# Optimization experiments

Hardware: AMD Instinct MI355X
Metric: run time of the kernel (lower is better)

## Reference

```python
import jax, jax.numpy as jnp
import numpy as np

B, S, H = 4, 2048, 1024
NH, HD = 16, 64
LN_EPS = 1e-5


def _l2norm(x, axis=-1, eps=1e-12):
    n = jnp.sqrt(jnp.sum(x * x, axis=axis, keepdims=True))
    return x / jnp.maximum(n, eps)


def setup_inputs() -> dict:
    key = jax.random.key(0)
    ks = jax.random.split(key, 10)
    sd = 0.02
    x = jax.random.normal(ks[0], (B, S, H), jnp.float32)
    Wq = jax.random.normal(ks[1], (H, H), jnp.float32) * sd
    Wk = jax.random.normal(ks[2], (H, H), jnp.float32) * sd
    Wv = jax.random.normal(ks[3], (H, H), jnp.float32) * sd
    Wa = jax.random.normal(ks[4], (NH, H), jnp.float32) * sd
    ba = jnp.zeros((NH,), jnp.float32)
    Wb = jax.random.normal(ks[5], (NH, H), jnp.float32) * sd
    bb = jnp.zeros((NH,), jnp.float32)
    Wg = jax.random.normal(ks[6], (H, H), jnp.float32) * sd
    Wo = jax.random.normal(ks[7], (H, H), jnp.float32) * sd
    ln_g = jnp.ones((H,), jnp.float32)
    ln_b = jnp.zeros((H,), jnp.float32)
    return {"x": x, "Wq": Wq, "Wk": Wk, "Wv": Wv, "Wa": Wa, "ba": ba,
            "Wb": Wb, "bb": bb, "Wg": Wg, "Wo": Wo, "ln_g": ln_g, "ln_b": ln_b}


def _forward(x, Wq, Wk, Wv, Wa, ba, Wb, bb, Wg, Wo, ln_g, ln_b):
    q = _l2norm((x @ Wq.T).reshape(B, S, NH, HD))  # [B,S,nh,hd]
    k = _l2norm((x @ Wk.T).reshape(B, S, NH, HD))
    v = jax.nn.silu(x @ Wv.T).reshape(B, S, NH, HD)
    alpha = jax.nn.sigmoid(x @ Wa.T + ba)  # [B,S,nh]
    beta = jax.nn.sigmoid(x @ Wb.T + bb)   # [B,S,nh]

    def step(state, inp):
        a_t, b_t, k_t, v_t, q_t = inp  # a,b: [B,nh]; k,v,q: [B,nh,hd]
        a_ = a_t[:, :, None, None]
        b_ = b_t[:, :, None, None]
        kk = k_t[..., :, None] * k_t[..., None, :]  # [B,nh,hd,hd]
        state = a_ * state * (1.0 - b_ * kk) + b_ * (v_t[..., :, None] * k_t[..., None, :])
        out_t = jnp.sum(state * q_t[..., None, :], axis=-1)  # [B,nh,hd]
        return state, out_t

    # time-major xs for scan
    xs = (jnp.moveaxis(alpha, 1, 0), jnp.moveaxis(beta, 1, 0),
          jnp.moveaxis(k, 1, 0), jnp.moveaxis(v, 1, 0), jnp.moveaxis(q, 1, 0))
    state0 = jnp.zeros((B, NH, HD, HD), x.dtype)
    _, outs = jax.lax.scan(step, state0, xs)  # [S,B,nh,hd]
    out = jnp.moveaxis(outs, 0, 1).reshape(B, S, H)

    # LayerNorm over total_dim
    mu = jnp.mean(out, axis=-1, keepdims=True)
    var = jnp.var(out, axis=-1, keepdims=True)
    out = (out - mu) / jnp.sqrt(var + LN_EPS) * ln_g + ln_b

    out = out * jax.nn.silu(x @ Wg.T)
    return out @ Wo.T


def reference(x, Wq, Wk, Wv, Wa, ba, Wb, bb, Wg, Wo, ln_g, ln_b):
    return _forward(x, Wq, Wk, Wv, Wa, ba, Wb, bb, Wg, Wo, ln_g, ln_b)
```

## Files before the change

kernel.cpp:

```cpp
#include <hip/hip_runtime.h>

typedef unsigned short u16;
typedef __bf16 bf16x8 __attribute__((ext_vector_type(8)));
typedef float f32x4 __attribute__((ext_vector_type(4)));

constexpr int Bq  = 4;
constexpr int Sq  = 2048;
constexpr int Hq  = 1024;
constexpr int NHq = 16;
constexpr int HDq = 64;
constexpr int CCH = 16;
constexpr int LCH = 128;

constexpr size_t OFF_WB = 0;
constexpr size_t OFF_XB = 10485760;
constexpr size_t OFF_Q  = 27262976;
constexpr size_t OFF_K  = 60817408;
constexpr size_t OFF_V  = 94371840;
constexpr size_t OFF_G  = 127926272;
constexpr size_t OFF_AL = 161480704;
constexpr size_t OFF_BE = 162004992;
constexpr size_t OFF_P  = 162529280;
constexpr size_t OFF_O  = 179306496;

__device__ __forceinline__ u16 f2bf(float f) {
  unsigned u = __float_as_uint(f);
  u += 0x7fffu + ((u >> 16) & 1u);
  return (u16)(u >> 16);
}
__device__ __forceinline__ float sigmoidf_(float x) { return 1.f / (1.f + __expf(-x)); }

__device__ __forceinline__ void async16(const void* g, void* l) {
  __builtin_amdgcn_global_load_lds((const __attribute__((address_space(1))) void*)g,
                                   (__attribute__((address_space(3))) void*)l, 16, 0, 0);
}

__global__ __launch_bounds__(256) void cvt_x_kernel(const float* __restrict__ in, u16* __restrict__ outp) {
  const size_t i = ((size_t)blockIdx.x * 256 + threadIdx.x) * 4;
  float4 f = *(const float4*)(in + i);
  ushort4 u; u.x = f2bf(f.x); u.y = f2bf(f.y); u.z = f2bf(f.z); u.w = f2bf(f.w);
  *(ushort4*)(outp + i) = u;
}

__global__ __launch_bounds__(256) void cvt_w_kernel(const float* __restrict__ w0, const float* __restrict__ w1,
    const float* __restrict__ w2, const float* __restrict__ w3, const float* __restrict__ w4,
    u16* __restrict__ outp) {
  const int z = blockIdx.z;
  const float* src = (z == 0) ? w0 : (z == 1) ? w1 : (z == 2) ? w2 : (z == 3) ? w3 : w4;
  const size_t i = ((size_t)blockIdx.x * 256 + threadIdx.x) * 4;
  float4 f = *(const float4*)(src + i);
  ushort4 u; u.x = f2bf(f.x); u.y = f2bf(f.y); u.z = f2bf(f.z); u.w = f2bf(f.w);
  *(ushort4*)(outp + (size_t)z * (1024 * 1024) + i) = u;
}

__global__ __launch_bounds__(256) void cvt_ab_kernel(const float* __restrict__ Wa, const float* __restrict__ Wb,
    u16* __restrict__ outp) {
  const size_t i = ((size_t)blockIdx.x * 256 + threadIdx.x) * 4;
  const int row = (int)(i >> 10);
  const float* src = (row < 16) ? (Wa + i) : (Wb + i - 16 * 1024);
  float4 f = *(const float4*)src;
  ushort4 u; u.x = f2bf(f.x); u.y = f2bf(f.y); u.z = f2bf(f.z); u.w = f2bf(f.w);
  *(ushort4*)(outp + i) = u;
}

__global__ __launch_bounds__(256) void ab_gemm(const u16* __restrict__ A, const u16* __restrict__ Wab,
    float* __restrict__ al, float* __restrict__ be, const float* __restrict__ ba, const float* __restrict__ bb) {
  const int tid = threadIdx.x, wv = tid >> 6, lane = tid & 63;
  const int l15 = lane & 15, qd = lane >> 4;
  const int m0 = blockIdx.x * 128 + wv * 32;
  const u16* gA = A + (size_t)m0 * 1024 + qd * 8;
  const u16* gB = Wab + (size_t)l15 * 1024 + qd * 8;
  f32x4 acc[2][2] = {};
#pragma unroll 4
  for (int kt = 0; kt < 1024; kt += 32) {
    bf16x8 a0 = *(const bf16x8*)(gA + (size_t)l15 * 1024 + kt);
    bf16x8 a1 = *(const bf16x8*)(gA + (size_t)(16 + l15) * 1024 + kt);
    bf16x8 b0 = *(const bf16x8*)(gB + kt);
    bf16x8 b1 = *(const bf16x8*)(gB + 16 * 1024 + kt);
    acc[0][0] = __builtin_amdgcn_mfma_f32_16x16x32_bf16(a0, b0, acc[0][0], 0, 0, 0);
    acc[0][1] = __builtin_amdgcn_mfma_f32_16x16x32_bf16(a0, b1, acc[0][1], 0, 0, 0);
    acc[1][0] = __builtin_amdgcn_mfma_f32_16x16x32_bf16(a1, b0, acc[1][0], 0, 0, 0);
    acc[1][1] = __builtin_amdgcn_mfma_f32_16x16x32_bf16(a1, b1, acc[1][1], 0, 0, 0);
  }
  const float bav = ba[l15], bbv = bb[l15];
#pragma unroll
  for (int mi = 0; mi < 2; ++mi) {
    const int row = m0 + mi * 16 + qd * 4;
#pragma unroll
    for (int r = 0; r < 4; ++r) {
      al[(size_t)(row + r) * 16 + l15] = sigmoidf_(acc[mi][0][r] + bav);
      be[(size_t)(row + r) * 16 + l15] = sigmoidf_(acc[mi][1][r] + bbv);
    }
  }
}

__device__ __forceinline__ void lda4(bf16x8 af[4][2], const u16* LA, int wr, int mh, int l15, int qd, int l7) {
#pragma unroll
  for (int i = 0; i < 4; ++i)
#pragma unroll
    for (int kk = 0; kk < 2; ++kk)
      af[i][kk] = *(const bf16x8*)(LA + (wr * 128 + mh * 64 + i * 16 + l15) * 64 + (((kk * 4 + qd) ^ l7) * 8));
}
__device__ __forceinline__ void ldb2(bf16x8 bf[2][2], const u16* LB, int wc, int nh, int l15, int qd, int l7) {
#pragma unroll
  for (int j = 0; j < 2; ++j)
#pragma unroll
    for (int kk = 0; kk < 2; ++kk)
      bf[j][kk] = *(const bf16x8*)(LB + (wc * 64 + nh * 32 + j * 16 + l15) * 64 + (((kk * 4 + qd) ^ l7) * 8));
}
__device__ __forceinline__ void mm16(f32x4 acc[8][4], const bf16x8 af[4][2], const bf16x8 bf[2][2], int mh, int nh) {
#pragma unroll
  for (int i = 0; i < 4; ++i)
#pragma unroll
    for (int j = 0; j < 2; ++j) {
      f32x4 c = acc[mh * 4 + i][nh * 2 + j];
      c = __builtin_amdgcn_mfma_f32_16x16x32_bf16(af[i][0], bf[j][0], c, 0, 0, 0);
      c = __builtin_amdgcn_mfma_f32_16x16x32_bf16(af[i][1], bf[j][1], c, 0, 0, 0);
      acc[mh * 4 + i][nh * 2 + j] = c;
    }
}
__device__ __forceinline__ void stageH(u16* LD, int bufp, int mat, int h, const u16* gRow0, int kElem,
                                       int rr, int sl8, int wv) {
  const u16* s0 = gRow0 + (size_t)(h * 128 + rr) * 1024 + kElem + sl8;
  u16* d = LD + bufp * 32768 + mat * 16384 + h * 8192 + wv * 512;
  async16(s0, d);
  async16(s0 + (size_t)(64 * 1024), d + 4096);
}

template<int S1, int S2, int VM>
__device__ __forceinline__ void tile16(u16* LD, int bp, int kt,
    const u16* gA, const u16* gB, f32x4 acc[8][4], bf16x8 af[4][2], bf16x8 bf0[2][2], bf16x8 bf1[2][2],
    int wr, int wc, int l15, int qd, int l7, int rr, int sl8, int wv) {
  const u16* LA = LD + bp * 32768;
  const u16* LB = LA + 16384;
  lda4(af, LA, wr, 0, l15, qd, l7);
  ldb2(bf0, LB, wc, 0, l15, qd, l7);
  if (S1) stageH(LD, bp ^ 1, 0, 0, gA, (kt + 1) * 64, rr, sl8, wv);
  __builtin_amdgcn_s_barrier();
  asm volatile("s_waitcnt lgkmcnt(0)" ::: "memory");
  __builtin_amdgcn_sched_barrier(0);
  __builtin_amdgcn_s_setprio(1);
  mm16(acc, af, bf0, 0, 0);
  __builtin_amdgcn_s_setprio(0);
  __builtin_amdgcn_s_barrier();
  ldb2(bf1, LB, wc, 1, l15, qd, l7);
  if (S1) stageH(LD, bp ^ 1, 0, 1, gA, (kt + 1) * 64, rr, sl8, wv);
  __builtin_amdgcn_s_barrier();
  asm volatile("s_waitcnt lgkmcnt(0)" ::: "memory");
  __builtin_amdgcn_sched_barrier(0);
  __builtin_amdgcn_s_setprio(1);
  mm16(acc, af, bf1, 0, 1);
  __builtin_amdgcn_s_setprio(0);
  __builtin_amdgcn_s_barrier();
  lda4(af, LA, wr, 1, l15, qd, l7);
  if (S2) stageH(LD, bp, 1, 0, gB, (kt + 2) * 64, rr, sl8, wv);
  __builtin_amdgcn_s_barrier();
  asm volatile("s_waitcnt lgkmcnt(0)" ::: "memory");
  __builtin_amdgcn_sched_barrier(0);
  __builtin_amdgcn_s_setprio(1);
  mm16(acc, af, bf0, 1, 0);
  __builtin_amdgcn_s_setprio(0);
  __builtin_amdgcn_s_barrier();
  if (S2) stageH(LD, bp, 1, 1, gB, (kt + 2) * 64, rr, sl8, wv);
  __builtin_amdgcn_s_barrier();
  __builtin_amdgcn_sched_barrier(0);
  __builtin_amdgcn_s_setprio(1);
  mm16(acc, af, bf1, 1, 1);
  __builtin_amdgcn_s_setprio(0);
  if (VM == 4) asm volatile("s_waitcnt vmcnt(4)" ::: "memory");
  else if (VM == 0) asm volatile("s_waitcnt vmcnt(0)" ::: "memory");
  __builtin_amdgcn_s_barrier();
}

__global__ __launch_bounds__(512, 2) void gemm256(const u16* __restrict__ A, const u16* __restrict__ Wall,
    float* __restrict__ Cq, float* __restrict__ Ck, float* __restrict__ Cv, float* __restrict__ Cg,
    int mode) {
  __shared__ __align__(16) u16 Lds[65536];
  u16* LD = &Lds[0];
  const int tid = threadIdx.x;
  const int wv = tid >> 6, lane = tid & 63;
  const int l15 = lane & 15, qd = lane >> 4, l7 = l15 & 7;
  const int wr = wv >> 2, wc = wv & 3;
  const int rr = tid >> 3, sl8 = ((tid & 7) ^ (rr & 7)) * 8;

  int mx, ny, z;
  const u16* Wm;
  if (mode == 0) {
    const int job = ((blockIdx.x & 7) << 4) + (blockIdx.x >> 3);
    mx = job & 31; ny = job >> 5; z = 0; Wm = Wall;
  } else {
    const int job = ((blockIdx.x & 7) << 6) + (blockIdx.x >> 3);
    mx = job & 31; ny = (job >> 5) & 3; z = job >> 7;
    Wm = Wall + (size_t)z * (1024 * 1024);
  }
  const int m0 = mx * 256, n0 = ny * 256;
  const u16* gA = A + (size_t)m0 * 1024;
  const u16* gB = Wm + (size_t)n0 * 1024;

  f32x4 acc[8][4] = {};
  bf16x8 af[4][2], bf0[2][2], bf1[2][2];

  stageH(LD, 0, 0, 0, gA, 0,  rr, sl8, wv);
  stageH(LD, 0, 0, 1, gA, 0,  rr, sl8, wv);
  stageH(LD, 0, 1, 0, gB, 0,  rr, sl8, wv);
  stageH(LD, 0, 1, 1, gB, 0,  rr, sl8, wv);
  stageH(LD, 1, 1, 0, gB, 64, rr, sl8, wv);
  stageH(LD, 1, 1, 1, gB, 64, rr, sl8, wv);
  asm volatile("s_waitcnt vmcnt(4)" ::: "memory");
  __builtin_amdgcn_s_barrier();

#pragma unroll 1
  for (int t2 = 0; t2 < 7; ++t2) {
    tile16<1, 1, 4>(LD, 0, 2 * t2,     gA, gB, acc, af, bf0, bf1, wr, wc, l15, qd, l7, rr, sl8, wv);
    tile16<1, 1, 4>(LD, 1, 2 * t2 + 1, gA, gB, acc, af, bf0, bf1, wr, wc, l15, qd, l7, rr, sl8, wv);
  }
  tile16<1, 0, 0>(LD, 0, 14, gA, gB, acc, af, bf0, bf1, wr, wc, l15, qd, l7, rr, sl8, wv);
  tile16<0, 0, -1>(LD, 1, 15, gA, gB, acc, af, bf0, bf1, wr, wc, l15, qd, l7, rr, sl8, wv);

  if (mode == 1 && z <= 1) {
#pragma unroll
    for (int mi = 0; mi < 8; ++mi)
#pragma unroll
      for (int r = 0; r < 4; ++r) {
        float ss = acc[mi][0][r] * acc[mi][0][r] + acc[mi][1][r] * acc[mi][1][r]
                 + acc[mi][2][r] * acc[mi][2][r] + acc[mi][3][r] * acc[mi][3][r];
        ss += __shfl_xor(ss, 1); ss += __shfl_xor(ss, 2);
        ss += __shfl_xor(ss, 4); ss += __shfl_xor(ss, 8);
        const float rn = 1.f / fmaxf(sqrtf(ss), 1e-12f);
        acc[mi][0][r] *= rn; acc[mi][1][r] *= rn; acc[mi][2][r] *= rn; acc[mi][3][r] *= rn;
      }
  } else if (mode == 1 && z == 2) {
#pragma unroll
    for (int mi = 0; mi < 8; ++mi)
#pragma unroll
      for (int ni = 0; ni < 4; ++ni)
#pragma unroll
        for (int r = 0; r < 4; ++r)
          acc[mi][ni][r] = acc[mi][ni][r] * sigmoidf_(acc[mi][ni][r]);
  }
  float* C = (mode == 0) ? Cq : ((z == 0) ? Cq : (z == 1) ? Ck : (z == 2) ? Cv : Cg);
#pragma unroll
  for (int mi = 0; mi < 8; ++mi) {
    const int row = m0 + wr * 128 + mi * 16 + qd * 4;
#pragma unroll
    for (int ni = 0; ni < 4; ++ni) {
      const int col = n0 + wc * 64 + ni * 16 + l15;
#pragma unroll
      for (int r = 0; r < 4; ++r)
        C[(size_t)(row + r) * 1024 + col] = acc[mi][ni][r];
    }
  }
}

struct ScanLds1 { float kb[2][16 * 64]; float vb[2][16 * 64]; float ab[2][32]; };
struct ScanLds2 { float kb[2][16 * 64]; float qb[2][16 * 64]; float vb[2][16 * 64]; float ab[2][32]; };

__global__ __launch_bounds__(256, 4) void scan_p1(const float* __restrict__ k, const float* __restrict__ v,
    const float* __restrict__ al, const float* __restrict__ be,
    float* __restrict__ P, float* __restrict__ Q) {
  __shared__ ScanLds1 L;
  const int tid = threadIdx.x, wv = tid >> 6, lane = tid & 63;
  const int bh = blockIdx.x >> 4, c = blockIdx.x & 15;
  const int b = bh >> 4, h = bh & 15;
  const int rg = lane >> 3, cg = lane & 7;
  const int r0 = wv * 16 + rg * 2, c8 = cg * 8;
  const size_t base0 = ((size_t)(b * Sq + c * LCH)) * 1024 + h * 64;
  const size_t ab0   = ((size_t)(b * Sq + c * LCH)) * 16 + h;
  const int tokw = lane >> 4, seg = lane & 15;
  auto stage = [&](int tile, int bi) {
    #pragma unroll
    for (int j = 0; j < 2; ++j) {
      const int job = wv * 2 + j;
      const int arr = job >> 2, i = job & 3;
      const float* src = arr ? v : k;
      float* dst = arr ? &L.vb[bi][i * 256] : &L.kb[bi][i * 256];
      async16(src + base0 + (size_t)(tile * 16 + i * 4 + tokw) * 1024 + seg * 4, dst);
    }
    if (wv == 0 && lane < 32) {
      const int w16 = lane >> 4, tt = lane & 15;
      const float* s = w16 ? be : al;
      L.ab[bi][w16 * 16 + tt] = s[ab0 + (size_t)(tile * 16 + tt) * 16];
    }
  };
  float Pr[16], Qr[16];
  #pragma unroll
  for (int i = 0; i < 16; ++i) { Pr[i] = 1.f; Qr[i] = 0.f; }
  stage(0, 0);
  for (int tile = 0; tile < 8; ++tile) {
    __syncthreads();
    if (tile < 7) stage(tile + 1, (tile + 1) & 1);
    const int bi = tile & 1;
    const float* kbp = L.kb[bi];
    const float* vbp = L.vb[bi];
    const float* abp = L.ab[bi];
    #pragma unroll 4
    for (int tt = 0; tt < 16; ++tt) {
      const float a = abp[tt], bt = abp[16 + tt];
      float4 kcv0 = *(const float4*)(kbp + tt * 64 + c8);
      float4 kcv1 = *(const float4*)(kbp + tt * 64 + c8 + 4);
      float2 krvv = *(const float2*)(kbp + tt * 64 + r0);
      float2 vrvv = *(const float2*)(vbp + tt * 64 + r0);
      const float kcv[8] = {kcv0.x, kcv0.y, kcv0.z, kcv0.w, kcv1.x, kcv1.y, kcv1.z, kcv1.w};
      const float krv[2] = {krvv.x, krvv.y};
      const float vrv[2] = {vrvv.x, vrvv.y};
      const float abt = a * bt;
      float c1[2], c2[2];
      #pragma unroll
      for (int i = 0; i < 2; ++i) { c1[i] = abt * krv[i]; c2[i] = bt * vrv[i]; }
      #pragma unroll
      for (int i = 0; i < 2; ++i)
        #pragma unroll
        for (int j = 0; j < 8; ++j) {
          const int e = i * 8 + j;
          const float A = fmaf(-c1[i], kcv[j], a);
          Qr[e] = fmaf(A, Qr[e], c2[i] * kcv[j]);
          Pr[e] *= A;
        }
    }
  }
  const size_t pbase = ((size_t)bh * CCH + c) * 4096 + (size_t)c8;
  #pragma unroll
  for (int i = 0; i < 2; ++i) {
    const size_t pi = pbase + (size_t)(r0 + i) * 64;
    *(float4*)(P + pi)     = make_float4(Pr[i*8],   Pr[i*8+1], Pr[i*8+2], Pr[i*8+3]);
    *(float4*)(P + pi + 4) = make_float4(Pr[i*8+4], Pr[i*8+5], Pr[i*8+6], Pr[i*8+7]);
    *(float4*)(Q + pi)     = make_float4(Qr[i*8],   Qr[i*8+1], Qr[i*8+2], Qr[i*8+3]);
    *(float4*)(Q + pi + 4) = make_float4(Qr[i*8+4], Qr[i*8+5], Qr[i*8+6], Qr[i*8+7]);
  }
}

__global__ __launch_bounds__(256) void scan_comb(float* __restrict__ P, const float* __restrict__ Q) {
  const int g = blockIdx.x * 256 + threadIdx.x;
  const int elem = g & 4095;
  const int bh = g >> 12;
  float s = 0.f;
  #pragma unroll
  for (int c = 0; c < CCH; ++c) {
    const size_t idx = ((size_t)bh * CCH + c) * 4096 + elem;
    const float p = P[idx], qq = Q[idx];
    P[idx] = s;
    s = fmaf(p, s, qq);
  }
}

__global__ __launch_bounds__(256, 4) void scan_p2(const float* __restrict__ q, const float* __restrict__ k,
    const float* __restrict__ v, const float* __restrict__ al, const float* __restrict__ be,
    const float* __restrict__ Pini, float* __restrict__ o) {
  __shared__ ScanLds2 L;
  const int tid = threadIdx.x, wv = tid >> 6, lane = tid & 63;
  const int bh = blockIdx.x >> 4, c = blockIdx.x & 15;
  const int b = bh >> 4, h = bh & 15;
  const int rg = lane >> 3, cg = lane & 7;
  const int r0 = wv * 16 + rg * 2, c8 = cg * 8;
  const size_t base0 = ((size_t)(b * Sq + c * LCH)) * 1024 + h * 64;
  const size_t ab0   = ((size_t)(b * Sq + c * LCH)) * 16 + h;
  const size_t pbase = ((size_t)bh * CCH + c) * 4096 + (size_t)c8;
  const int tokw = lane >> 4, seg = lane & 15;
  auto stage = [&](int tile, int bi) {
    #pragma unroll
    for (int j = 0; j < 3; ++j) {
      const int job = wv * 3 + j;
      const int arr = job >> 2, i = job & 3;
      const float* src = (arr == 0) ? k : (arr == 1) ? q : v;
      float* dst = (arr == 0) ? &L.kb[bi][i * 256] : (arr == 1) ? &L.qb[bi][i * 256]
                                                                : &L.vb[bi][i * 256];
      async16(src + base0 + (size_t)(tile * 16 + i * 4 + tokw) * 1024 + seg * 4, dst);
    }
    if (wv == 0 && lane < 32) {
      const int w16 = lane >> 4, tt = lane & 15;
      const float* s = w16 ? be : al;
      L.ab[bi][w16 * 16 + tt] = s[ab0 + (size_t)(tile * 16 + tt) * 16];
    }
  };
  float st[16];
  #pragma unroll
  for (int i = 0; i < 2; ++i) {
    float4 s0 = *(const float4*)(Pini + pbase + (size_t)(r0 + i) * 64);
    float4 s1 = *(const float4*)(Pini + pbase + (size_t)(r0 + i) * 64 + 4);
    st[i*8]   = s0.x; st[i*8+1] = s0.y; st[i*8+2] = s0.z; st[i*8+3] = s0.w;
    st[i*8+4] = s1.x; st[i*8+5] = s1.y; st[i*8+6] = s1.z; st[i*8+7] = s1.w;
  }
  stage(0, 0);
  const bool hi4 = (cg & 4);
  const int rowIdx = r0 + (cg >> 2);
  const bool doStore = ((cg & 3) == 0);
  for (int tile = 0; tile < 8; ++tile) {
    __syncthreads();
    if (tile < 7) stage(tile + 1, (tile + 1) & 1);
    const int bi = tile & 1;
    const float* kbp = L.kb[bi];
    const float* qbp = L.qb[bi];
    const float* vbp = L.vb[bi];
    const float* abp = L.ab[bi];
    #pragma unroll 2
    for (int tt = 0; tt < 16; ++tt) {
      const int t = tile * 16 + tt;
      const float a = abp[tt], bt = abp[16 + tt];
      float4 kc0 = *(const float4*)(kbp + tt * 64 + c8);
      float4 kc1 = *(const float4*)(kbp + tt * 64 + c8 + 4);
      float4 qc0 = *(const float4*)(qbp + tt * 64 + c8);
      float4 qc1 = *(const float4*)(qbp + tt * 64 + c8 + 4);
      float2 krvv = *(const float2*)(kbp + tt * 64 + r0);
      float2 vrvv = *(const float2*)(vbp + tt * 64 + r0);
      const float kcv[8] = {kc0.x, kc0.y, kc0.z, kc0.w, kc1.x, kc1.y, kc1.z, kc1.w};
      const float qcv[8] = {qc0.x, qc0.y, qc0.z, qc0.w, qc1.x, qc1.y, qc1.z, qc1.w};
      const float krv[2] = {krvv.x, krvv.y};
      const float vrv[2] = {vrvv.x, vrvv.y};
      const float abt = a * bt;
      float c1[2], c2[2];
      #pragma unroll
      for (int i = 0; i < 2; ++i) { c1[i] = abt * krv[i]; c2[i] = bt * vrv[i]; }
      float p[2];
      p[0] = 0.f; p[1] = 0.f;
      #pragma unroll
      for (int i = 0; i < 2; ++i)
        #pragma unroll
        for (int j = 0; j < 8; ++j) {
          const int e = i * 8 + j;
          const float A = fmaf(-c1[i], kcv[j], a);
          st[e] = fmaf(A, st[e], c2[i] * kcv[j]);
          p[i] = fmaf(st[e], qcv[j], p[i]);
        }
      float my    = hi4 ? p[1] : p[0];
      float other = hi4 ? p[0] : p[1];
      my += __shfl_xor(other, 4);
      my += __shfl_xor(my, 2);
      my += __shfl_xor(my, 1);
      if (doStore) o[base0 + (size_t)t * 1024 + rowIdx] = my;
    }
  }
}

__global__ __launch_bounds__(256) void ln_gate_kernel(const float* __restrict__ o, const float* __restrict__ g,
    const float* __restrict__ ln_g, const float* __restrict__ ln_b, u16* __restrict__ y) {
  const int t = blockIdx.x, tid = threadIdx.x;
  const size_t row = (size_t)t * 1024;
  float4 xv = *(const float4*)(o + row + tid * 4);
  float s  = xv.x + xv.y + xv.z + xv.w;
  float s2 = xv.x * xv.x + xv.y * xv.y + xv.z * xv.z + xv.w * xv.w;
  #pragma unroll
  for (int m = 1; m < 64; m <<= 1) { s += __shfl_xor(s, m); s2 += __shfl_xor(s2, m); }
  __shared__ float red[8];
  const int w = tid >> 6, lane = tid & 63;
  if (lane == 0) { red[w] = s; red[4 + w] = s2; }
  __syncthreads();
  s  = red[0] + red[1] + red[2] + red[3];
  s2 = red[4] + red[5] + red[6] + red[7];
  const float mu = s * (1.f / 1024.f);
  const float var = s2 * (1.f / 1024.f) - mu * mu;
  const float rstd = rsqrtf(var + 1e-5f);
  float4 gv = *(const float4*)(g + row + tid * 4);
  float4 lg = *(const float4*)(ln_g + tid * 4);
  float4 lb = *(const float4*)(ln_b + tid * 4);
  ushort4 u;
  u.x = f2bf(((xv.x - mu) * rstd * lg.x + lb.x) * (gv.x * sigmoidf_(gv.x)));
  u.y = f2bf(((xv.y - mu) * rstd * lg.y + lb.y) * (gv.y * sigmoidf_(gv.y)));
  u.z = f2bf(((xv.z - mu) * rstd * lg.z + lb.z) * (gv.z * sigmoidf_(gv.z)));
  u.w = f2bf(((xv.w - mu) * rstd * lg.w + lb.w) * (gv.w * sigmoidf_(gv.w)));
  *(ushort4*)(y + row + tid * 4) = u;
}

extern "C" void kernel_launch(void* const* d_in, const int* in_sizes, int n_in,
                              void* d_out, int out_size, void* d_ws, size_t ws_size,
                              hipStream_t stream) {
  const float* x    = (const float*)d_in[0];
  const float* Wq   = (const float*)d_in[1];
  const float* Wk   = (const float*)d_in[2];
  const float* Wv   = (const float*)d_in[3];
  const float* Wa   = (const float*)d_in[4];
  const float* ba   = (const float*)d_in[5];
  const float* Wb   = (const float*)d_in[6];
  const float* bb   = (const float*)d_in[7];
  const float* Wg   = (const float*)d_in[8];
  const float* Wo   = (const float*)d_in[9];
  const float* ln_g = (const float*)d_in[10];
  const float* ln_b = (const float*)d_in[11];
  float* out = (float*)d_out;
  char* ws = (char*)d_ws;

  u16*   wb  = (u16*)(ws + OFF_WB);
  u16*   xb  = (u16*)(ws + OFF_XB);
  float* qf  = (float*)(ws + OFF_Q);
  float* kf  = (float*)(ws + OFF_K);
  float* vf  = (float*)(ws + OFF_V);
  float* gf  = (float*)(ws + OFF_G);
  float* al  = (float*)(ws + OFF_AL);
  float* be  = (float*)(ws + OFF_BE);
  u16*   wab = (u16*)(ws + OFF_P);
  float* Pb  = (float*)(ws + OFF_P);
  float* Qc  = (float*)(ws + OFF_XB);
  float* of  = (float*)(ws + OFF_O);
  u16*   yb  = xb;

  cvt_x_kernel<<<8192, 256, 0, stream>>>(x, xb);
  cvt_w_kernel<<<dim3(1024, 1, 5), 256, 0, stream>>>(Wq, Wk, Wv, Wg, Wo, wb);
  cvt_ab_kernel<<<32, 256, 0, stream>>>(Wa, Wb, wab);
  ab_gemm<<<64, 256, 0, stream>>>(xb, wab, al, be, ba, bb);
  gemm256<<<512, 512, 0, stream>>>(xb, wb, qf, kf, vf, gf, 1);
  scan_p1<<<1024, 256, 0, stream>>>(kf, vf, al, be, Pb, Qc);
  scan_comb<<<1024, 256, 0, stream>>>(Pb, Qc);
  scan_p2<<<1024, 256, 0, stream>>>(qf, kf, vf, al, be, Pb, of);
  ln_gate_kernel<<<8192, 256, 0, stream>>>(of, gf, ln_g, ln_b, yb);
  gemm256<<<128, 512, 0, stream>>>(yb, wb + (size_t)4 * 1024 * 1024, out, out, out, out, 0);
}
```

Baseline: 419.2 us.

## Store q/k/v/gate projections as bf16 and expand in LDS inside scans

New measurement: 454.6 us. 1.08x slower.

```diff
diff --git a/kernel.cpp b/kernel.cpp
--- a/kernel.cpp
+++ b/kernel.cpp
@@ -15,19 +15,20 @@
 constexpr size_t OFF_WB = 0;
 constexpr size_t OFF_XB = 10485760;
 constexpr size_t OFF_Q  = 27262976;
-constexpr size_t OFF_K  = 60817408;
-constexpr size_t OFF_V  = 94371840;
-constexpr size_t OFF_G  = 127926272;
-constexpr size_t OFF_AL = 161480704;
-constexpr size_t OFF_BE = 162004992;
-constexpr size_t OFF_P  = 162529280;
-constexpr size_t OFF_O  = 179306496;
+constexpr size_t OFF_K  = 44040192;
+constexpr size_t OFF_V  = 60817408;
+constexpr size_t OFF_G  = 77594624;
+constexpr size_t OFF_AL = 94371840;
+constexpr size_t OFF_BE = 94896128;
+constexpr size_t OFF_P  = 95420416;
+constexpr size_t OFF_O  = 112197632;
 
 __device__ __forceinline__ u16 f2bf(float f) {
   unsigned u = __float_as_uint(f);
   u += 0x7fffu + ((u >> 16) & 1u);
   return (u16)(u >> 16);
 }
+__device__ __forceinline__ float bf2f(u16 h) { return __uint_as_float((unsigned)h << 16); }
 __device__ __forceinline__ float sigmoidf_(float x) { return 1.f / (1.f + __expf(-x)); }
 
 __device__ __forceinline__ void async16(const void* g, void* l) {
@@ -173,8 +174,8 @@
 }
 
 __global__ __launch_bounds__(512, 2) void gemm256(const u16* __restrict__ A, const u16* __restrict__ Wall,
-    float* __restrict__ Cq, float* __restrict__ Ck, float* __restrict__ Cv, float* __restrict__ Cg,
-    int mode) {
+    float* __restrict__ C0, u16* __restrict__ q16, u16* __restrict__ k16, u16* __restrict__ v16,
+    u16* __restrict__ g16, int mode) {
   __shared__ __align__(16) u16 Lds[65536];
   u16* LD = &Lds[0];
   const int tid = threadIdx.x;
@@ -186,11 +187,10 @@
   int mx, ny, z;
   const u16* Wm;
   if (mode == 0) {
-    const int job = ((blockIdx.x & 7) << 4) + (blockIdx.x >> 3);
-    mx = job & 31; ny = job >> 5; z = 0; Wm = Wall;
+    mx = blockIdx.x & 31; ny = blockIdx.x >> 5; z = 0; Wm = Wall;
   } else {
-    const int job = ((blockIdx.x & 7) << 6) + (blockIdx.x >> 3);
-    mx = job & 31; ny = (job >> 5) & 3; z = job >> 7;
+    const int b = blockIdx.x;
+    mx = b & 31; ny = (b >> 5) & 3; z = b >> 7;
     Wm = Wall + (size_t)z * (1024 * 1024);
   }
   const int m0 = mx * 256, n0 = ny * 256;
@@ -217,7 +217,21 @@
   tile16<1, 0, 0>(LD, 0, 14, gA, gB, acc, af, bf0, bf1, wr, wc, l15, qd, l7, rr, sl8, wv);
   tile16<0, 0, -1>(LD, 1, 15, gA, gB, acc, af, bf0, bf1, wr, wc, l15, qd, l7, rr, sl8, wv);
 
-  if (mode == 1 && z <= 1) {
+  if (mode == 0) {
+#pragma unroll
+    for (int mi = 0; mi < 8; ++mi) {
+      const int row = m0 + wr * 128 + mi * 16 + qd * 4;
+#pragma unroll
+      for (int ni = 0; ni < 4; ++ni) {
+        const int col = n0 + wc * 64 + ni * 16 + l15;
+#pragma unroll
+        for (int r = 0; r < 4; ++r)
+          C0[(size_t)(row + r) * 1024 + col] = acc[mi][ni][r];
+      }
+    }
+    return;
+  }
+  if (z <= 1) {
 #pragma unroll
     for (int mi = 0; mi < 8; ++mi)
 #pragma unroll
@@ -229,7 +243,7 @@
         const float rn = 1.f / fmaxf(sqrtf(ss), 1e-12f);
         acc[mi][0][r] *= rn; acc[mi][1][r] *= rn; acc[mi][2][r] *= rn; acc[mi][3][r] *= rn;
       }
-  } else if (mode == 1 && z == 2) {
+  } else if (z == 2) {
 #pragma unroll
     for (int mi = 0; mi < 8; ++mi)
 #pragma unroll
@@ -238,7 +252,7 @@
         for (int r = 0; r < 4; ++r)
           acc[mi][ni][r] = acc[mi][ni][r] * sigmoidf_(acc[mi][ni][r]);
   }
-  float* C = (mode == 0) ? Cq : ((z == 0) ? Cq : (z == 1) ? Ck : (z == 2) ? Cv : Cg);
+  u16* C16 = (z == 0) ? q16 : (z == 1) ? k16 : (z == 2) ? v16 : g16;
 #pragma unroll
   for (int mi = 0; mi < 8; ++mi) {
     const int row = m0 + wr * 128 + mi * 16 + qd * 4;
@@ -247,15 +261,33 @@
       const int col = n0 + wc * 64 + ni * 16 + l15;
 #pragma unroll
       for (int r = 0; r < 4; ++r)
-        C[(size_t)(row + r) * 1024 + col] = acc[mi][ni][r];
-    }
-  }
-}
-
-struct ScanLds1 { float kb[2][16 * 64]; float vb[2][16 * 64]; float ab[2][32]; };
-struct ScanLds2 { float kb[2][16 * 64]; float qb[2][16 * 64]; float vb[2][16 * 64]; float ab[2][32]; };
-
-__global__ __launch_bounds__(256, 4) void scan_p1(const float* __restrict__ k, const float* __restrict__ v,
+        C16[(size_t)(row + r) * 1024 + col] = f2bf(acc[mi][ni][r]);
+    }
+  }
+}
+
+struct ScanLds1 {
+  float kb[2][1024]; float vb[2][1024];
+  u16   kb16[2][1024]; u16 vb16[2][1024];
+  float ab[2][32];
+};
+struct ScanLds2 {
+  float kb[2][1024]; float qb[2][1024]; float vb[2][1024];
+  u16   kb16[2][1024]; u16 qb16[2][1024]; u16 vb16[2][1024];
+  float ab[2][32];
+};
+
+__device__ __forceinline__ void expand4(const u16* src16, float* dstf, int tid) {
+  uint2 w = *(const uint2*)(src16 + tid * 4);
+  float4 f;
+  f.x = __uint_as_float(w.x << 16);
+  f.y = __uint_as_float(w.x & 0xffff0000u);
+  f.z = __uint_as_float(w.y << 16);
+  f.w = __uint_as_float(w.y & 0xffff0000u);
+  *(float4*)(dstf + tid * 4) = f;
+}
+
+__global__ __launch_bounds__(256, 4) void scan_p1(const u16* __restrict__ k, const u16* __restrict__ v,
     const float* __restrict__ al, const float* __restrict__ be,
     float* __restrict__ P, float* __restrict__ Q) {
   __shared__ ScanLds1 L;
@@ -266,16 +298,12 @@
   const int r0 = wv * 16 + rg * 2, c8 = cg * 8;
   const size_t base0 = ((size_t)(b * Sq + c * LCH)) * 1024 + h * 64;
   const size_t ab0   = ((size_t)(b * Sq + c * LCH)) * 16 + h;
-  const int tokw = lane >> 4, seg = lane & 15;
+  const int trow = lane >> 3, colg = (lane & 7) * 8;
   auto stage = [&](int tile, int bi) {
-    #pragma unroll
-    for (int j = 0; j < 2; ++j) {
-      const int job = wv * 2 + j;
-      const int arr = job >> 2, i = job & 3;
-      const float* src = arr ? v : k;
-      float* dst = arr ? &L.vb[bi][i * 256] : &L.kb[bi][i * 256];
-      async16(src + base0 + (size_t)(tile * 16 + i * 4 + tokw) * 1024 + seg * 4, dst);
-    }
+    const int arr = wv >> 1, hh = wv & 1;
+    const u16* src = arr ? v : k;
+    u16* dst = (arr ? &L.vb16[bi][0] : &L.kb16[bi][0]) + hh * 512;
+    async16(src + base0 + (size_t)(tile * 16 + hh * 8 + trow) * 1024 + colg, dst);
     if (wv == 0 && lane < 32) {
       const int w16 = lane >> 4, tt = lane & 15;
       const float* s = w16 ? be : al;
@@ -288,8 +316,11 @@
   stage(0, 0);
   for (int tile = 0; tile < 8; ++tile) {
     __syncthreads();
-    if (tile < 7) stage(tile + 1, (tile + 1) & 1);
     const int bi = tile & 1;
+    if (tile < 7) stage(tile + 1, bi ^ 1);
+    expand4(&L.kb16[bi][0], &L.kb[bi][0], tid);
+    expand4(&L.vb16[bi][0], &L.vb[bi][0], tid);
+    __syncthreads();
     const float* kbp = L.kb[bi];
     const float* vbp = L.vb[bi];
     const float* abp = L.ab[bi];
@@ -343,8 +374,8 @@
   }
 }
 
-__global__ __launch_bounds__(256, 4) void scan_p2(const float* __restrict__ q, const float* __restrict__ k,
-    const float* __restrict__ v, const float* __restrict__ al, const float* __restrict__ be,
+__global__ __launch_bounds__(256, 4) void scan_p2(const u16* __restrict__ q, const u16* __restrict__ k,
+    const u16* __restrict__ v, const float* __restrict__ al, const float* __restrict__ be,
     const float* __restrict__ Pini, float* __restrict__ o) {
   __shared__ ScanLds2 L;
   const int tid = threadIdx.x, wv = tid >> 6, lane = tid & 63;
@@ -355,18 +386,19 @@
   const size_t base0 = ((size_t)(b * Sq + c * LCH)) * 1024 + h * 64;
   const size_t ab0   = ((size_t)(b * Sq + c * LCH)) * 16 + h;
   const size_t pbase = ((size_t)bh * CCH + c) * 4096 + (size_t)c8;
-  const int tokw = lane >> 4, seg = lane & 15;
+  const int trow = lane >> 3, colg = (lane & 7) * 8;
   auto stage = [&](int tile, int bi) {
     #pragma unroll
-    for (int j = 0; j < 3; ++j) {
-      const int job = wv * 3 + j;
-      const int arr = job >> 2, i = job & 3;
-      const float* src = (arr == 0) ? k : (arr == 1) ? q : v;
-      float* dst = (arr == 0) ? &L.kb[bi][i * 256] : (arr == 1) ? &L.qb[bi][i * 256]
-                                                                : &L.vb[bi][i * 256];
-      async16(src + base0 + (size_t)(tile * 16 + i * 4 + tokw) * 1024 + seg * 4, dst);
-    }
-    if (wv == 0 && lane < 32) {
+    for (int jj = 0; jj < 2; ++jj) {
+      const int job = wv + jj * 4;
+      if (job < 6) {
+        const int arr = job >> 1, hh = job & 1;
+        const u16* src = (arr == 0) ? k : (arr == 1) ? q : v;
+        u16* dst = ((arr == 0) ? &L.kb16[bi][0] : (arr == 1) ? &L.qb16[bi][0] : &L.vb16[bi][0]) + hh * 512;
+        async16(src + base0 + (size_t)(tile * 16 + hh * 8 + trow) * 1024 + colg, dst);
+      }
+    }
+    if (wv == 2 && lane < 32) {
       const int w16 = lane >> 4, tt = lane & 15;
       const float* s = w16 ? be : al;
       L.ab[bi][w16 * 16 + tt] = s[ab0 + (size_t)(tile * 16 + tt) * 16];
@@ -386,8 +418,12 @@
   const bool doStore = ((cg & 3) == 0);
   for (int tile = 0; tile < 8; ++tile) {
     __syncthreads();
-    if (tile < 7) stage(tile + 1, (tile + 1) & 1);
     const int bi = tile & 1;
+    if (tile < 7) stage(tile + 1, bi ^ 1);
+    expand4(&L.kb16[bi][0], &L.kb[bi][0], tid);
+    expand4(&L.qb16[bi][0], &L.qb[bi][0], tid);
+    expand4(&L.vb16[bi][0], &L.vb[bi][0], tid);
+    __syncthreads();
     const float* kbp = L.kb[bi];
     const float* qbp = L.qb[bi];
     const float* vbp = L.vb[bi];
@@ -431,7 +467,7 @@
   }
 }
 
-__global__ __launch_bounds__(256) void ln_gate_kernel(const float* __restrict__ o, const float* __restrict__ g,
+__global__ __launch_bounds__(256) void ln_gate_kernel(const float* __restrict__ o, const u16* __restrict__ g16,
     const float* __restrict__ ln_g, const float* __restrict__ ln_b, u16* __restrict__ y) {
   const int t = blockIdx.x, tid = threadIdx.x;
   const size_t row = (size_t)t * 1024;
@@ -449,14 +485,15 @@
   const float mu = s * (1.f / 1024.f);
   const float var = s2 * (1.f / 1024.f) - mu * mu;
   const float rstd = rsqrtf(var + 1e-5f);
-  float4 gv = *(const float4*)(g + row + tid * 4);
+  ushort4 gv4 = *(const ushort4*)(g16 + row + tid * 4);
+  const float gx = bf2f(gv4.x), gy = bf2f(gv4.y), gz = bf2f(gv4.z), gw = bf2f(gv4.w);
   float4 lg = *(const float4*)(ln_g + tid * 4);
   float4 lb = *(const float4*)(ln_b + tid * 4);
   ushort4 u;
-  u.x = f2bf(((xv.x - mu) * rstd * lg.x + lb.x) * (gv.x * sigmoidf_(gv.x)));
-  u.y = f2bf(((xv.y - mu) * rstd * lg.y + lb.y) * (gv.y * sigmoidf_(gv.y)));
-  u.z = f2bf(((xv.z - mu) * rstd * lg.z + lb.z) * (gv.z * sigmoidf_(gv.z)));
-  u.w = f2bf(((xv.w - mu) * rstd * lg.w + lb.w) * (gv.w * sigmoidf_(gv.w)));
+  u.x = f2bf(((xv.x - mu) * rstd * lg.x + lb.x) * (gx * sigmoidf_(gx)));
+  u.y = f2bf(((xv.y - mu) * rstd * lg.y + lb.y) * (gy * sigmoidf_(gy)));
+  u.z = f2bf(((xv.z - mu) * rstd * lg.z + lb.z) * (gz * sigmoidf_(gz)));
+  u.w = f2bf(((xv.w - mu) * rstd * lg.w + lb.w) * (gw * sigmoidf_(gw)));
   *(ushort4*)(y + row + tid * 4) = u;
 }
 
@@ -480,10 +517,10 @@
 
   u16*   wb  = (u16*)(ws + OFF_WB);
   u16*   xb  = (u16*)(ws + OFF_XB);
-  float* qf  = (float*)(ws + OFF_Q);
-  float* kf  = (float*)(ws + OFF_K);
-  float* vf  = (float*)(ws + OFF_V);
-  float* gf  = (float*)(ws + OFF_G);
+  u16*   qb16 = (u16*)(ws + OFF_Q);
+  u16*   kb16 = (u16*)(ws + OFF_K);
+  u16*   vb16 = (u16*)(ws + OFF_V);
+  u16*   gb16 = (u16*)(ws + OFF_G);
   float* al  = (float*)(ws + OFF_AL);
   float* be  = (float*)(ws + OFF_BE);
   u16*   wab = (u16*)(ws + OFF_P);
@@ -496,10 +533,10 @@
   cvt_w_kernel<<<dim3(1024, 1, 5), 256, 0, stream>>>(Wq, Wk, Wv, Wg, Wo, wb);
   cvt_ab_kernel<<<32, 256, 0, stream>>>(Wa, Wb, wab);
   ab_gemm<<<64, 256, 0, stream>>>(xb, wab, al, be, ba, bb);
-  gemm256<<<512, 512, 0, stream>>>(xb, wb, qf, kf, vf, gf, 1);
-  scan_p1<<<1024, 256, 0, stream>>>(kf, vf, al, be, Pb, Qc);
+  gemm256<<<512, 512, 0, stream>>>(xb, wb, nullptr, qb16, kb16, vb16, gb16, 1);
+  scan_p1<<<1024, 256, 0, stream>>>(kb16, vb16, al, be, Pb, Qc);
   scan_comb<<<1024, 256, 0, stream>>>(Pb, Qc);
-  scan_p2<<<1024, 256, 0, stream>>>(qf, kf, vf, al, be, Pb, of);
-  ln_gate_kernel<<<8192, 256, 0, stream>>>(of, gf, ln_g, ln_b, yb);
-  gemm256<<<128, 512, 0, stream>>>(yb, wb + (size_t)4 * 1024 * 1024, out, out, out, out, 0);
-}
+  scan_p2<<<1024, 256, 0, stream>>>(qb16, kb16, vb16, al, be, Pb, of);
+  ln_gate_kernel<<<8192, 256, 0, stream>>>(of, gb16, ln_g, ln_b, yb);
+  gemm256<<<128, 512, 0, stream>>>(yb, wb + (size_t)4 * 1024 * 1024, out, nullptr, nullptr, nullptr, nullptr, 0);
+}
```
